# Optimization experiments

Hardware: AMD Instinct MI355X
Metric: run time of the kernel (lower is better)

Reference implementation:

```python
import jax, jax.numpy as jnp
import numpy as np

EPS = 1e-08


def setup_inputs() -> dict:
    key = jax.random.key(0)
    X = jax.random.normal(key, (16384, 768), dtype=jnp.float32)
    return {"X": X}


def reference(X) -> jnp.ndarray:
    # L2-normalize rows (torch F.normalize with eps: divide by max(norm, eps))
    norms = jnp.linalg.norm(X, axis=-1, keepdims=True)
    Xn = X / jnp.maximum(norms, EPS)

    n = Xn.shape[0]
    # pairwise inner products [n, n]; mask self-similarity on diagonal with -1
    dots = Xn @ Xn.T
    dots = jnp.where(jnp.eye(n, dtype=bool), jnp.float32(-1.0), dots)
    I = jnp.argmax(dots, axis=1)  # nearest neighbor index per row

    # torch PairwiseDistance(2, eps): ||x - y + eps||_2
    diff = Xn - Xn[I] + EPS
    distances = jnp.linalg.norm(diff, axis=-1)

    # loss_type == 'standard'
    loss = -jnp.mean(jnp.log(distances + EPS))
    return loss
```

## Files before the change

kernel.cpp:

```cpp
#include <hip/hip_runtime.h>
#include <hip/hip_bf16.h>
#include <stdint.h>
#include <math.h>

#define NR 16384
#define DIM 768
#define KEPS 1e-8f

#define BM 128
#define NB (NR / BM)
#define KT (DIM / 64)
#define NQ (DIM / 16)
#define NTILES (NB * (NB + 1) / 2)

typedef __attribute__((ext_vector_type(4))) float f32x4;
typedef __attribute__((ext_vector_type(2))) long long2_t;

__device__ inline uint32_t fkey(float f) {
    union { float f; uint32_t u; } v; v.f = f;
    return (v.u & 0x80000000u) ? ~v.u : (v.u | 0x80000000u);
}

__device__ inline unsigned long long pack_vc(float v, int c) {
    return ((unsigned long long)fkey(v) << 32) | (unsigned)c;
}

__device__ inline uint8_t f2fp8(float f) {
    union { float f; uint32_t u; } v; v.f = f;
    const uint8_t s = (uint8_t)((v.u >> 24) & 0x80u);
    float a = fabsf(f);
    if (a >= 448.0f) return s | 0x7E;
    if (a < 0.015625f) {
        int q = (int)rintf(a * 512.0f);
        if (q >= 8) return s | 0x08;
        return s | (uint8_t)q;
    }
    int ex; float m = frexpf(a, &ex);
    int E = ex + 6;
    int frac = (int)rintf(m * 16.0f - 8.0f);
    if (frac >= 8) { frac = 0; ++E; if (E > 15) return s | 0x7E; }
    return s | (uint8_t)(E << 3) | (uint8_t)frac;
}

__global__ __launch_bounds__(256) void k_norm(const float* __restrict__ X,
                                              uint8_t* __restrict__ XnT,
                                              float* __restrict__ norms) {
    __shared__ uint8_t buf[4][768];
    const int wid = threadIdx.x >> 6, lane = threadIdx.x & 63;
    const int row = blockIdx.x * 4 + wid;
    const float4* xr = (const float4*)(X + (size_t)row * DIM) + lane * 3;
    float4 a = xr[0], b = xr[1], c = xr[2];
    float s = a.x*a.x + a.y*a.y + a.z*a.z + a.w*a.w
            + b.x*b.x + b.y*b.y + b.z*b.z + b.w*b.w
            + c.x*c.x + c.y*c.y + c.z*c.z + c.w*c.w;
#pragma unroll
    for (int m = 32; m >= 1; m >>= 1) s += __shfl_xor(s, m);
    const float n = sqrtf(s);
    if (lane == 0) norms[row] = n;
    const float rn = 1.0f / fmaxf(n, KEPS);
    float v[12] = {a.x,a.y,a.z,a.w,b.x,b.y,b.z,b.w,c.x,c.y,c.z,c.w};
    uint8_t q[12];
#pragma unroll
    for (int i = 0; i < 12; ++i) q[i] = f2fp8(v[i] * rn);
    uint32_t* lb = (uint32_t*)&buf[wid][lane * 12];
    lb[0] = (uint32_t)q[0] | ((uint32_t)q[1] << 8) | ((uint32_t)q[2]  << 16) | ((uint32_t)q[3]  << 24);
    lb[1] = (uint32_t)q[4] | ((uint32_t)q[5] << 8) | ((uint32_t)q[6]  << 16) | ((uint32_t)q[7]  << 24);
    lb[2] = (uint32_t)q[8] | ((uint32_t)q[9] << 8) | ((uint32_t)q[10] << 16) | ((uint32_t)q[11] << 24);
    __syncthreads();
    if (lane < NQ) {
        const int blk = lane >> 2;
        const int h   = lane & 3;
        const uint2 lo = *(const uint2*)&buf[wid][blk * 64 + h * 8];
        const uint2 hi = *(const uint2*)&buf[wid][blk * 64 + 32 + h * 8];
        const size_t off = ((size_t)(row >> 7) * NQ * 128 + (size_t)lane * 128
                            + (row & 127)) * 16;
        *(uint4*)(XnT + off) = make_uint4(lo.x, lo.y, hi.x, hi.y);
    }
}

__global__ __launch_bounds__(256) void k_init(unsigned long long* __restrict__ nn64) {
    nn64[blockIdx.x * 256 + threadIdx.x] = pack_vc(-2.0f, 0);
}

__global__ __launch_bounds__(256, 4) void k_maxdot(const uint8_t* __restrict__ XnT,
                                                   unsigned long long* __restrict__ nn64) {
    const int tid  = threadIdx.x;
    const int lane = tid & 63, wid = tid >> 6;
    const int wr = wid >> 1, wc = wid & 1;
    const int l15 = lane & 15, lhi = lane >> 4;

    int t = (int)blockIdx.x;
    t = (t & 7) * (NTILES / 8) + (t >> 3);
    float disc = 66049.0f - 8.0f * (float)t;
    int rb = (int)((257.0f - sqrtf(disc)) * 0.5f);
    if (rb > NB - 1) rb = NB - 1;
    if (rb < 0) rb = 0;
    while (rb > 0 && rb * (257 - rb) / 2 > t) --rb;
    while ((rb + 1) * (257 - (rb + 1)) / 2 <= t) ++rb;
    const int cb = rb + (t - rb * (257 - rb) / 2);
    const int rowbase = rb * BM;
    const int colbase = cb * BM;
    const bool diag = (rb == cb);

    const uint8_t* pA = XnT + (size_t)rb * NQ * 128 * 16;
    const uint8_t* pB = XnT + (size_t)cb * NQ * 128 * 16;

    f32x4 acc[4][4];
    const f32x4 z = {0.f, 0.f, 0.f, 0.f};
#pragma unroll
    for (int i = 0; i < 4; ++i)
#pragma unroll
        for (int j = 0; j < 4; ++j) acc[i][j] = z;

    const int arow = wr * 64 + l15;
    const int brow = wc * 64 + l15;
#pragma unroll 2
    for (int kt = 0; kt < KT; ++kt) {
        const size_t qoff = (size_t)(kt * 4 + lhi) * 128 * 16;
        long2_t af[4], bg[4];
#pragma unroll
        for (int mf = 0; mf < 4; ++mf)
            af[mf] = *(const long2_t*)(pA + qoff + (size_t)(arow + mf * 16) * 16);
#pragma unroll
        for (int nf = 0; nf < 4; ++nf)
            bg[nf] = *(const long2_t*)(pB + qoff + (size_t)(brow + nf * 16) * 16);
#pragma unroll
        for (int mf = 0; mf < 4; ++mf)
#pragma unroll
            for (int nf = 0; nf < 4; ++nf)
                acc[mf][nf] = __builtin_amdgcn_mfma_f32_16x16x32_fp8_fp8(
                    af[mf].x, bg[nf].x, acc[mf][nf], 0, 0, 0);
#pragma unroll
        for (int mf = 0; mf < 4; ++mf)
#pragma unroll
            for (int nf = 0; nf < 4; ++nf)
                acc[mf][nf] = __builtin_amdgcn_mfma_f32_16x16x32_fp8_fp8(
                    af[mf].y, bg[nf].y, acc[mf][nf], 0, 0, 0);
    }

    if (diag) {
#pragma unroll
        for (int mf = 0; mf < 4; ++mf)
#pragma unroll
            for (int nf = 0; nf < 4; ++nf)
#pragma unroll
                for (int rr = 0; rr < 4; ++rr) {
                    const int rl = wr * 64 + mf * 16 + lhi * 4 + rr;
                    const int cl = wc * 64 + nf * 16 + l15;
                    if (rl == cl) acc[mf][nf][rr] = -1.0f;
                }
    }

#pragma unroll
    for (int mf = 0; mf < 4; ++mf)
#pragma unroll
        for (int rr = 0; rr < 4; ++rr) {
            float v = acc[mf][0][rr];
            int   c = colbase + wc * 64 + l15;
#pragma unroll
            for (int nf = 1; nf < 4; ++nf) {
                const float w2 = acc[mf][nf][rr];
                const int   c2 = colbase + wc * 64 + nf * 16 + l15;
                if (w2 > v) { v = w2; c = c2; }
            }
#pragma unroll
            for (int m = 1; m <= 8; m <<= 1) {
                const float ov = __shfl_xor(v, m);
                const int   oc = __shfl_xor(c, m);
                if (ov > v) { v = ov; c = oc; }
            }
            if (l15 == 0) {
                const int r = rowbase + wr * 64 + mf * 16 + lhi * 4 + rr;
                atomicMax(&nn64[r], pack_vc(v, c));
            }
        }

#pragma unroll
    for (int nf = 0; nf < 4; ++nf) {
        float v = acc[0][nf][0];
        int   c = rowbase + wr * 64 + lhi * 4;
#pragma unroll
        for (int mf = 0; mf < 4; ++mf)
#pragma unroll
            for (int rr = 0; rr < 4; ++rr) {
                if (mf == 0 && rr == 0) continue;
                const float w2 = acc[mf][nf][rr];
                const int   c2 = rowbase + wr * 64 + mf * 16 + lhi * 4 + rr;
                if (w2 > v) { v = w2; c = c2; }
            }
#pragma unroll
        for (int m = 16; m <= 32; m <<= 1) {
            const float ov = __shfl_xor(v, m);
            const int   oc = __shfl_xor(c, m);
            if (ov > v) { v = ov; c = oc; }
        }
        if ((lane >> 4) == 0) {
            const int cc = colbase + wc * 64 + nf * 16 + l15;
            atomicMax(&nn64[cc], pack_vc(v, c));
        }
    }
}

__global__ __launch_bounds__(256) void k_refine(const float* __restrict__ X,
                                                const float* __restrict__ norms,
                                                const unsigned long long* __restrict__ nn64,
                                                float* __restrict__ logd) {
    const int wid = threadIdx.x >> 6, lane = threadIdx.x & 63;
    const int r = blockIdx.x * 4 + wid;
    const int j = (int)(nn64[r] & 0xFFFFu);
    const float rnr = 1.0f / fmaxf(norms[r], KEPS);
    const float rnj = 1.0f / fmaxf(norms[j], KEPS);
    const float4* xr = (const float4*)(X + (size_t)r * DIM) + lane * 3;
    const float4* xj = (const float4*)(X + (size_t)j * DIM) + lane * 3;
    float s = 0.0f;
#pragma unroll
    for (int i = 0; i < 3; ++i) {
        const float4 a = xr[i], b = xj[i];
        float d;
        d = a.x * rnr - b.x * rnj + KEPS; s = fmaf(d, d, s);
        d = a.y * rnr - b.y * rnj + KEPS; s = fmaf(d, d, s);
        d = a.z * rnr - b.z * rnj + KEPS; s = fmaf(d, d, s);
        d = a.w * rnr - b.w * rnj + KEPS; s = fmaf(d, d, s);
    }
#pragma unroll
    for (int m = 32; m >= 1; m >>= 1) s += __shfl_xor(s, m);
    if (lane == 0) logd[r] = logf(sqrtf(s) + KEPS);
}

__global__ __launch_bounds__(256) void k_loss(const float* __restrict__ logd,
                                              float* __restrict__ out) {
    float local = 0.0f;
    for (int r = threadIdx.x; r < NR; r += 256) local += logd[r];
#pragma unroll
    for (int m = 32; m >= 1; m >>= 1) local += __shfl_xor(local, m);
    __shared__ float red[4];
    const int lane = threadIdx.x & 63, wid = threadIdx.x >> 6;
    if (lane == 0) red[wid] = local;
    __syncthreads();
    if (threadIdx.x == 0)
        out[0] = -(red[0] + red[1] + red[2] + red[3]) / (float)NR;
}

extern "C" void kernel_launch(void* const* d_in, const int* in_sizes, int n_in,
                              void* d_out, int out_size, void* d_ws, size_t ws_size,
                              hipStream_t stream) {
    const float* X = (const float*)d_in[0];
    float* out = (float*)d_out;
    uint8_t* XnT = (uint8_t*)d_ws;
    char* p = (char*)d_ws + (size_t)NR * DIM;
    float* norms = (float*)p;                 p += (size_t)NR * 4;
    unsigned long long* nn64 = (unsigned long long*)p; p += (size_t)NR * 8;
    float* logd = (float*)p;

    k_norm<<<NR / 4, 256, 0, stream>>>(X, XnT, norms);
    k_init<<<NR / 256, 256, 0, stream>>>(nn64);
    k_maxdot<<<NTILES, 256, 0, stream>>>(XnT, nn64);
    k_refine<<<NR / 4, 256, 0, stream>>>(X, norms, nn64, logd);
    k_loss<<<1, 256, 0, stream>>>(logd, out);
}
```

Measured before the change: 307.5 us.

## Enlarge maxdot block tile to 256x128 with 128x64 per-warp fragments

Each block of the upper-triangular similarity search now covers a 256-row by 128-column tile instead of 128x128, and each wave computes a 128x64 sub-tile. The tile-index to (row, col) mapping is redone for the new triangular shape, and the diagonal masking uses global row/column indices. The aim is to issue more FP8 MFMAs per fragment loaded from global memory, which cuts load traffic per unit of compute. In exchange the accumulators double, occupancy is lowered to two blocks per unit, and some blocks next to the diagonal compute a little redundant work.

```diff
diff --git a/kernel.cpp b/kernel.cpp
--- a/kernel.cpp
+++ b/kernel.cpp
@@ -7,11 +7,10 @@
 #define DIM 768
 #define KEPS 1e-8f
 
-#define BM 128
-#define NB (NR / BM)
+#define NB 128
 #define KT (DIM / 64)
 #define NQ (DIM / 16)
-#define NTILES (NB * (NB + 1) / 2)
+#define NTILES 4160
 
 typedef __attribute__((ext_vector_type(4))) float f32x4;
 typedef __attribute__((ext_vector_type(2))) long long2_t;
@@ -82,7 +81,7 @@
     nn64[blockIdx.x * 256 + threadIdx.x] = pack_vc(-2.0f, 0);
 }
 
-__global__ __launch_bounds__(256, 4) void k_maxdot(const uint8_t* __restrict__ XnT,
+__global__ __launch_bounds__(256, 2) void k_maxdot(const uint8_t* __restrict__ XnT,
                                                    unsigned long long* __restrict__ nn64) {
     const int tid  = threadIdx.x;
     const int lane = tid & 63, wid = tid >> 6;
@@ -91,76 +90,75 @@
 
     int t = (int)blockIdx.x;
     t = (t & 7) * (NTILES / 8) + (t >> 3);
-    float disc = 66049.0f - 8.0f * (float)t;
-    int rb = (int)((257.0f - sqrtf(disc)) * 0.5f);
-    if (rb > NB - 1) rb = NB - 1;
+    int rb = (int)((129.0f - sqrtf(16641.0f - 4.0f * (float)t)) * 0.5f);
     if (rb < 0) rb = 0;
-    while (rb > 0 && rb * (257 - rb) / 2 > t) --rb;
-    while ((rb + 1) * (257 - (rb + 1)) / 2 <= t) ++rb;
-    const int cb = rb + (t - rb * (257 - rb) / 2);
-    const int rowbase = rb * BM;
-    const int colbase = cb * BM;
-    const bool diag = (rb == cb);
-
-    const uint8_t* pA = XnT + (size_t)rb * NQ * 128 * 16;
+    if (rb > 63) rb = 63;
+    while (rb > 0 && rb * (129 - rb) > t) --rb;
+    while ((rb + 1) * (129 - (rb + 1)) <= t) ++rb;
+    const int cb = 2 * rb + (t - rb * (129 - rb));
+
+    const uint8_t* pA = XnT + (size_t)(2 * rb + wr) * NQ * 128 * 16;
     const uint8_t* pB = XnT + (size_t)cb * NQ * 128 * 16;
-
-    f32x4 acc[4][4];
+    const int rowbase = rb * 256 + wr * 128;
+    const int colbase = cb * 128 + wc * 64;
+    const bool maybe_diag = (cb == 2 * rb) || (cb == 2 * rb + 1);
+
+    f32x4 acc[8][4];
     const f32x4 z = {0.f, 0.f, 0.f, 0.f};
 #pragma unroll
-    for (int i = 0; i < 4; ++i)
+    for (int i = 0; i < 8; ++i)
 #pragma unroll
         for (int j = 0; j < 4; ++j) acc[i][j] = z;
 
-    const int arow = wr * 64 + l15;
+    const int arow = l15;
     const int brow = wc * 64 + l15;
 #pragma unroll 2
     for (int kt = 0; kt < KT; ++kt) {
         const size_t qoff = (size_t)(kt * 4 + lhi) * 128 * 16;
-        long2_t af[4], bg[4];
-#pragma unroll
-        for (int mf = 0; mf < 4; ++mf)
+        long2_t af[8], bg[4];
+#pragma unroll
+        for (int mf = 0; mf < 8; ++mf)
             af[mf] = *(const long2_t*)(pA + qoff + (size_t)(arow + mf * 16) * 16);
 #pragma unroll
         for (int nf = 0; nf < 4; ++nf)
             bg[nf] = *(const long2_t*)(pB + qoff + (size_t)(brow + nf * 16) * 16);
 #pragma unroll
-        for (int mf = 0; mf < 4; ++mf)
+        for (int mf = 0; mf < 8; ++mf)
 #pragma unroll
             for (int nf = 0; nf < 4; ++nf)
                 acc[mf][nf] = __builtin_amdgcn_mfma_f32_16x16x32_fp8_fp8(
                     af[mf].x, bg[nf].x, acc[mf][nf], 0, 0, 0);
 #pragma unroll
-        for (int mf = 0; mf < 4; ++mf)
+        for (int mf = 0; mf < 8; ++mf)
 #pragma unroll
             for (int nf = 0; nf < 4; ++nf)
                 acc[mf][nf] = __builtin_amdgcn_mfma_f32_16x16x32_fp8_fp8(
                     af[mf].y, bg[nf].y, acc[mf][nf], 0, 0, 0);
     }
 
-    if (diag) {
-#pragma unroll
-        for (int mf = 0; mf < 4; ++mf)
+    if (maybe_diag) {
+#pragma unroll
+        for (int mf = 0; mf < 8; ++mf)
 #pragma unroll
             for (int nf = 0; nf < 4; ++nf)
 #pragma unroll
                 for (int rr = 0; rr < 4; ++rr) {
-                    const int rl = wr * 64 + mf * 16 + lhi * 4 + rr;
-                    const int cl = wc * 64 + nf * 16 + l15;
+                    const int rl = rowbase + mf * 16 + lhi * 4 + rr;
+                    const int cl = colbase + nf * 16 + l15;
                     if (rl == cl) acc[mf][nf][rr] = -1.0f;
                 }
     }
 
 #pragma unroll
-    for (int mf = 0; mf < 4; ++mf)
+    for (int mf = 0; mf < 8; ++mf)
 #pragma unroll
         for (int rr = 0; rr < 4; ++rr) {
             float v = acc[mf][0][rr];
-            int   c = colbase + wc * 64 + l15;
+            int   c = colbase + l15;
 #pragma unroll
             for (int nf = 1; nf < 4; ++nf) {
                 const float w2 = acc[mf][nf][rr];
-                const int   c2 = colbase + wc * 64 + nf * 16 + l15;
+                const int   c2 = colbase + nf * 16 + l15;
                 if (w2 > v) { v = w2; c = c2; }
             }
 #pragma unroll
@@ -170,7 +168,7 @@
                 if (ov > v) { v = ov; c = oc; }
             }
             if (l15 == 0) {
-                const int r = rowbase + wr * 64 + mf * 16 + lhi * 4 + rr;
+                const int r = rowbase + mf * 16 + lhi * 4 + rr;
                 atomicMax(&nn64[r], pack_vc(v, c));
             }
         }
@@ -178,14 +176,14 @@
 #pragma unroll
     for (int nf = 0; nf < 4; ++nf) {
         float v = acc[0][nf][0];
-        int   c = rowbase + wr * 64 + lhi * 4;
-#pragma unroll
-        for (int mf = 0; mf < 4; ++mf)
+        int   c = rowbase + lhi * 4;
+#pragma unroll
+        for (int mf = 0; mf < 8; ++mf)
 #pragma unroll
             for (int rr = 0; rr < 4; ++rr) {
                 if (mf == 0 && rr == 0) continue;
                 const float w2 = acc[mf][nf][rr];
-                const int   c2 = rowbase + wr * 64 + mf * 16 + lhi * 4 + rr;
+                const int   c2 = rowbase + mf * 16 + lhi * 4 + rr;
                 if (w2 > v) { v = w2; c = c2; }
             }
 #pragma unroll
@@ -195,7 +193,7 @@
             if (ov > v) { v = ov; c = oc; }
         }
         if ((lane >> 4) == 0) {
-            const int cc = colbase + wc * 64 + nf * 16 + l15;
+            const int cc = colbase + nf * 16 + l15;
             atomicMax(&nn64[cc], pack_vc(v, c));
         }
     }
```

New measurement: 299.7 us. 2.6% less time.
